# Performance work log

Measured on AMD Instinct MI355X. Metric: run time of the kernel, lower is better.

Reference implementation:

```python
import jax, jax.numpy as jnp
import numpy as np

SIGMA2 = 0.01       # inlier_params[0] -> Scorer_dist sigma2
INLIER_ALPHA = 0.5  # inlier_params[-1]


def setup_inputs() -> dict:
    key = jax.random.key(0)
    k1, k2, k3 = jax.random.split(key, 3)
    B, H, N = 32, 256, 8192
    pts = jax.random.normal(k1, (B, N, 3), dtype=jnp.float32)
    target = jax.random.normal(k2, (B, 3), dtype=jnp.float32)
    sample_idx = jax.random.randint(k3, (B, H, 3), 0, N)
    return {"pts": pts, "target": target, "sample_idx": sample_idx}


def _fit_planes(pts, sample_idx):
    # gather 3 points per hypothesis: pts [B,N,3], sample_idx [B,H,3] -> [B,H,3,3]
    B = pts.shape[0]
    b_idx = jnp.arange(B)[:, None, None]
    tri = pts[b_idx, sample_idx]                     # [B,H,3pts,3coords]
    p0, p1, p2 = tri[:, :, 0], tri[:, :, 1], tri[:, :, 2]
    n = jnp.cross(p1 - p0, p2 - p0)                  # plane normal [B,H,3]
    d = -jnp.sum(n * p0, axis=-1, keepdims=True)     # plane offset [B,H,1]
    planes = jnp.concatenate([n, d], axis=-1)        # [B,H,4]
    # sample_hyp fallback: degenerate (all-zero) planes replaced by ones
    all_zero = jnp.all(planes == 0, axis=-1, keepdims=True)
    planes = jnp.where(all_zero, jnp.ones_like(planes), planes)
    # normalize all 4 components by normal norm
    norm = jnp.sqrt(jnp.sum(planes[..., :3] ** 2, axis=-1, keepdims=True))
    return planes / norm


def reference(pts, target, sample_idx):
    B = pts.shape[0]
    planes = _fit_planes(pts, sample_idx)            # [B,H,4]
    normal = planes[..., :3]
    # Scorer_dist: |n . p + d| over all points, gaussian, sum over points
    dists = jnp.abs(jnp.einsum('bhc,bnc->bhn', normal, pts) + planes[..., 3:4])
    score = jnp.sum(jnp.exp(-(dists ** 2) / (2.0 * SIGMA2)), axis=2)  # [B,H]
    # ms_euclidean loss against target normal (sign-invariant)
    t = target[:, None, :]                           # [B,1,3]
    loss = jnp.minimum(jnp.sum((normal - t) ** 2, axis=2),
                       jnp.sum((normal + t) ** 2, axis=2))            # [B,H]
    maxidx = jnp.argmax(score, axis=1)               # [B]
    top_loss = jnp.take_along_axis(loss, maxidx[:, None], axis=1)[:, 0]
    pred = jnp.take_along_axis(normal, maxidx[:, None, None], axis=1)[:, 0]
    w = jax.nn.softmax(INLIER_ALPHA * score, axis=1)
    exp_loss = jnp.sum(loss * w, axis=1)             # [B]
    return exp_loss, top_loss, pred
```

## Files before the change

### kernel.cpp

```cpp
#include <hip/hip_runtime.h>
#include <math.h>

#define BB 32
#define HH 256
#define NN 8192
#define CC 16
#define CHUNK (NN / CC)
#define P 8
#define SUB (CHUNK / P)

#define WS_LOSS_F ((size_t)BB * HH * 4)
#define WS_PART_F (WS_LOSS_F + (size_t)BB * HH)

__global__ __launch_bounds__(HH) void score_kernel(
    const float* __restrict__ pts, const float* __restrict__ target,
    const int* __restrict__ sidx, float* __restrict__ ws,
    float* __restrict__ partial) {
  const int chunk = blockIdx.x, b = blockIdx.y;
  const int h = threadIdx.x;
  __shared__ float4 smp[CHUNK * 3 / 4];
  __shared__ float4 plane_lds[HH];
  __shared__ float scorepad[HH * 9];

  const float4* src4 =
      (const float4*)(pts + ((long)b * NN + (long)chunk * CHUNK) * 3);
#pragma unroll
  for (int j = h; j < CHUNK * 3 / 4; j += HH) {
    __builtin_amdgcn_global_load_lds(src4 + j, &smp[j], 16, 0, 0);
  }

  long ibase = ((long)b * HH + h) * 3;
  int i0 = sidx[ibase], i1 = sidx[ibase + 1], i2 = sidx[ibase + 2];
  const float* pb = pts + (long)b * NN * 3;
  float p0x = pb[3 * i0], p0y = pb[3 * i0 + 1], p0z = pb[3 * i0 + 2];
  float p1x = pb[3 * i1], p1y = pb[3 * i1 + 1], p1z = pb[3 * i1 + 2];
  float p2x = pb[3 * i2], p2y = pb[3 * i2 + 1], p2z = pb[3 * i2 + 2];
  float v1x = p1x - p0x, v1y = p1y - p0y, v1z = p1z - p0z;
  float v2x = p2x - p0x, v2y = p2y - p0y, v2z = p2z - p0z;
  float nx = __fsub_rn(__fmul_rn(v1y, v2z), __fmul_rn(v1z, v2y));
  float ny = __fsub_rn(__fmul_rn(v1z, v2x), __fmul_rn(v1x, v2z));
  float nz = __fsub_rn(__fmul_rn(v1x, v2y), __fmul_rn(v1y, v2x));
  float d = -(__fmul_rn(nx, p0x) + __fmul_rn(ny, p0y) + __fmul_rn(nz, p0z));
  if (nx == 0.0f && ny == 0.0f && nz == 0.0f && d == 0.0f) {
    nx = 1.0f; ny = 1.0f; nz = 1.0f; d = 1.0f;
  }
  float norm = sqrtf(nx * nx + ny * ny + nz * nz);
  nx /= norm; ny /= norm; nz /= norm; d /= norm;
  plane_lds[h] = make_float4(nx, ny, nz, d);

  if (chunk == 0) {
    ((float4*)ws)[b * HH + h] = make_float4(nx, ny, nz, d);
    float tx = target[b * 3], ty = target[b * 3 + 1], tz = target[b * 3 + 2];
    float lm = (nx - tx) * (nx - tx) + (ny - ty) * (ny - ty) + (nz - tz) * (nz - tz);
    float lp = (nx + tx) * (nx + tx) + (ny + ty) * (ny + ty) + (nz + tz) * (nz + tz);
    ws[WS_LOSS_F + b * HH + h] = fminf(lm, lp);
  }
  __syncthreads();

  const float SC = 8.4932180028801371f;
  const int pid = h & 31;
  const int s = h >> 5;
  float4 pls[P];
#pragma unroll
  for (int k = 0; k < P; ++k) {
    float4 q = plane_lds[pid + (k << 5)];
    pls[k] = make_float4(q.x * SC, q.y * SC, q.z * SC, q.w * SC);
  }

  float acc[P];
#pragma unroll
  for (int k = 0; k < P; ++k) acc[k] = 0.f;
  const int sbase = s * (SUB * 3 / 4);
#pragma unroll 4
  for (int g = 0; g < SUB / 4; ++g) {
    float4 v0 = smp[sbase + 3 * g + 0];
    float4 v1 = smp[sbase + 3 * g + 1];
    float4 v2 = smp[sbase + 3 * g + 2];
#pragma unroll
    for (int k = 0; k < P; ++k) {
      float4 q = pls[k];
      float t0 = fmaf(q.x, v0.x, fmaf(q.y, v0.y, fmaf(q.z, v0.z, q.w)));
      float t1 = fmaf(q.x, v0.w, fmaf(q.y, v1.x, fmaf(q.z, v1.y, q.w)));
      float t2 = fmaf(q.x, v1.z, fmaf(q.y, v1.w, fmaf(q.z, v2.x, q.w)));
      float t3 = fmaf(q.x, v2.y, fmaf(q.y, v2.z, fmaf(q.z, v2.w, q.w)));
      float e0 = __builtin_amdgcn_exp2f(-(t0 * t0));
      float e1 = __builtin_amdgcn_exp2f(-(t1 * t1));
      float e2 = __builtin_amdgcn_exp2f(-(t2 * t2));
      float e3 = __builtin_amdgcn_exp2f(-(t3 * t3));
      acc[k] += (e0 + e1) + (e2 + e3);
    }
  }

#pragma unroll
  for (int k = 0; k < P; ++k) scorepad[(pid + (k << 5)) * 9 + s] = acc[k];
  __syncthreads();
  float rowsum = 0.f;
#pragma unroll
  for (int j = 0; j < P; ++j) rowsum += scorepad[h * 9 + j];
  partial[((long)b * CC + chunk) * HH + h] = rowsum;
}

__global__ __launch_bounds__(HH) void finalize_kernel(
    const float* __restrict__ ws, float* __restrict__ out) {
  int b = blockIdx.x, h = threadIdx.x;
  const float* lossArr = ws + WS_LOSS_F;
  const float* partial = ws + WS_PART_F;
  float s = 0.f;
#pragma unroll
  for (int c = 0; c < CC; ++c) s += partial[((long)b * CC + c) * HH + h];
  float l = lossArr[b * HH + h];

  __shared__ float redv[4];
  __shared__ int redi[4];
  __shared__ float sw[4], swl[4];

  float v = s; int idx = h;
#pragma unroll
  for (int o = 32; o > 0; o >>= 1) {
    float ov = __shfl_xor(v, o);
    int oi = __shfl_xor(idx, o);
    if (ov > v || (ov == v && oi < idx)) { v = ov; idx = oi; }
  }
  const int wid = h >> 6;
  if ((h & 63) == 0) { redv[wid] = v; redi[wid] = idx; }
  __syncthreads();
  float m = redv[0]; int mi = redi[0];
#pragma unroll
  for (int w = 1; w < 4; ++w) {
    float ov = redv[w]; int oi = redi[w];
    if (ov > m || (ov == m && oi < mi)) { m = ov; mi = oi; }
  }

  const float HL = 0.72134752044448170f;
  float wv = __builtin_amdgcn_exp2f(HL * (s - m));
  float wl = wv * l;
#pragma unroll
  for (int o = 32; o > 0; o >>= 1) {
    wv += __shfl_xor(wv, o);
    wl += __shfl_xor(wl, o);
  }
  if ((h & 63) == 0) { sw[wid] = wv; swl[wid] = wl; }
  __syncthreads();
  if (h == 0) {
    float S1 = (sw[0] + sw[1]) + (sw[2] + sw[3]);
    float S2 = (swl[0] + swl[1]) + (swl[2] + swl[3]);
    out[b] = S2 / S1;
    out[BB + b] = lossArr[b * HH + mi];
    float4 p = ((const float4*)ws)[b * HH + mi];
    out[2 * BB + 3 * b + 0] = p.x;
    out[2 * BB + 3 * b + 1] = p.y;
    out[2 * BB + 3 * b + 2] = p.z;
  }
}

extern "C" void kernel_launch(void* const* d_in, const int* in_sizes, int n_in,
                              void* d_out, int out_size, void* d_ws, size_t ws_size,
                              hipStream_t stream) {
  const float* pts = (const float*)d_in[0];
  const float* target = (const float*)d_in[1];
  const int* sidx = (const int*)d_in[2];
  float* out = (float*)d_out;
  float* ws = (float*)d_ws;
  float* partial = ws + WS_PART_F;

  score_kernel<<<dim3(CC, BB), HH, 0, stream>>>(pts, target, sidx, ws, partial);
  finalize_kernel<<<BB, HH, 0, stream>>>(ws, out);
}
```

Baseline: 22.95 us.

## Split hypotheses across blocks and specialize warps for loading vs plane fitting

The grid is repartitioned from 16 point chunks into 8 chunks by 2 hypothesis halves. Each block now scores 128 planes against 1024 points, with P reduced to 4 planes per thread. Within a block, the upper 128 threads issue the async point-to-LDS copies while the lower 128 gather sample points and fit planes, so the two phases overlap. Normalization now uses a reciprocal sqrt instead of sqrt plus divides, which changes rounding slightly. The score accumulation now spans the whole 1024-point chunk per block, which raises the point data loaded per plane and could cost more memory traffic.

```diff
diff --git a/kernel.cpp b/kernel.cpp
--- a/kernel.cpp
+++ b/kernel.cpp
@@ -4,56 +4,67 @@
 #define BB 32
 #define HH 256
 #define NN 8192
-#define CC 16
-#define CHUNK (NN / CC)
-#define P 8
-#define SUB (CHUNK / P)
+#define NC 8
+#define PHALF 2
+#define CHUNK (NN / NC)
+#define PPB (HH / PHALF)
+#define P 4
+#define SUB (CHUNK / 8)
 
 #define WS_LOSS_F ((size_t)BB * HH * 4)
 #define WS_PART_F (WS_LOSS_F + (size_t)BB * HH)
 
-__global__ __launch_bounds__(HH) void score_kernel(
+__global__ __launch_bounds__(256) void score_kernel(
     const float* __restrict__ pts, const float* __restrict__ target,
     const int* __restrict__ sidx, float* __restrict__ ws,
     float* __restrict__ partial) {
-  const int chunk = blockIdx.x, b = blockIdx.y;
+  const int bx = blockIdx.x;
+  const int ph = bx >> 3, chunk = bx & 7;
+  const int b = blockIdx.y;
   const int h = threadIdx.x;
+
   __shared__ float4 smp[CHUNK * 3 / 4];
-  __shared__ float4 plane_lds[HH];
-  __shared__ float scorepad[HH * 9];
+  __shared__ float4 plane_lds[PPB];
+  __shared__ float scorepad[PPB * 9];
 
-  const float4* src4 =
-      (const float4*)(pts + ((long)b * NN + (long)chunk * CHUNK) * 3);
+  if (h >= 128) {
+    const float4* src4 =
+        (const float4*)(pts + ((long)b * NN + (long)chunk * CHUNK) * 3);
+    const int l = h - 128;
 #pragma unroll
-  for (int j = h; j < CHUNK * 3 / 4; j += HH) {
-    __builtin_amdgcn_global_load_lds(src4 + j, &smp[j], 16, 0, 0);
-  }
+    for (int i = 0; i < 6; ++i) {
+      __builtin_amdgcn_global_load_lds(src4 + l + 128 * i, &smp[l + 128 * i],
+                                       16, 0, 0);
+    }
+  } else {
+    long ibase = ((long)b * HH + ph * PPB + h) * 3;
+    int i0 = sidx[ibase], i1 = sidx[ibase + 1], i2 = sidx[ibase + 2];
+    const float* pb = pts + (long)b * NN * 3;
+    float p0x = pb[3 * i0], p0y = pb[3 * i0 + 1], p0z = pb[3 * i0 + 2];
+    float p1x = pb[3 * i1], p1y = pb[3 * i1 + 1], p1z = pb[3 * i1 + 2];
+    float p2x = pb[3 * i2], p2y = pb[3 * i2 + 1], p2z = pb[3 * i2 + 2];
+    float v1x = p1x - p0x, v1y = p1y - p0y, v1z = p1z - p0z;
+    float v2x = p2x - p0x, v2y = p2y - p0y, v2z = p2z - p0z;
+    float nx = __fsub_rn(__fmul_rn(v1y, v2z), __fmul_rn(v1z, v2y));
+    float ny = __fsub_rn(__fmul_rn(v1z, v2x), __fmul_rn(v1x, v2z));
+    float nz = __fsub_rn(__fmul_rn(v1x, v2y), __fmul_rn(v1y, v2x));
+    float d = -(__fmul_rn(nx, p0x) + __fmul_rn(ny, p0y) + __fmul_rn(nz, p0z));
+    if (nx == 0.0f && ny == 0.0f && nz == 0.0f && d == 0.0f) {
+      nx = 1.0f; ny = 1.0f; nz = 1.0f; d = 1.0f;
+    }
+    float inv = __builtin_amdgcn_rsqf(nx * nx + ny * ny + nz * nz);
+    nx *= inv; ny *= inv; nz *= inv; d *= inv;
+    plane_lds[h] = make_float4(nx, ny, nz, d);
 
-  long ibase = ((long)b * HH + h) * 3;
-  int i0 = sidx[ibase], i1 = sidx[ibase + 1], i2 = sidx[ibase + 2];
-  const float* pb = pts + (long)b * NN * 3;
-  float p0x = pb[3 * i0], p0y = pb[3 * i0 + 1], p0z = pb[3 * i0 + 2];
-  float p1x = pb[3 * i1], p1y = pb[3 * i1 + 1], p1z = pb[3 * i1 + 2];
-  float p2x = pb[3 * i2], p2y = pb[3 * i2 + 1], p2z = pb[3 * i2 + 2];
-  float v1x = p1x - p0x, v1y = p1y - p0y, v1z = p1z - p0z;
-  float v2x = p2x - p0x, v2y = p2y - p0y, v2z = p2z - p0z;
-  float nx = __fsub_rn(__fmul_rn(v1y, v2z), __fmul_rn(v1z, v2y));
-  float ny = __fsub_rn(__fmul_rn(v1z, v2x), __fmul_rn(v1x, v2z));
-  float nz = __fsub_rn(__fmul_rn(v1x, v2y), __fmul_rn(v1y, v2x));
-  float d = -(__fmul_rn(nx, p0x) + __fmul_rn(ny, p0y) + __fmul_rn(nz, p0z));
-  if (nx == 0.0f && ny == 0.0f && nz == 0.0f && d == 0.0f) {
-    nx = 1.0f; ny = 1.0f; nz = 1.0f; d = 1.0f;
-  }
-  float norm = sqrtf(nx * nx + ny * ny + nz * nz);
-  nx /= norm; ny /= norm; nz /= norm; d /= norm;
-  plane_lds[h] = make_float4(nx, ny, nz, d);
-
-  if (chunk == 0) {
-    ((float4*)ws)[b * HH + h] = make_float4(nx, ny, nz, d);
-    float tx = target[b * 3], ty = target[b * 3 + 1], tz = target[b * 3 + 2];
-    float lm = (nx - tx) * (nx - tx) + (ny - ty) * (ny - ty) + (nz - tz) * (nz - tz);
-    float lp = (nx + tx) * (nx + tx) + (ny + ty) * (ny + ty) + (nz + tz) * (nz + tz);
-    ws[WS_LOSS_F + b * HH + h] = fminf(lm, lp);
+    if (chunk == 0) {
+      ((float4*)ws)[b * HH + ph * PPB + h] = make_float4(nx, ny, nz, d);
+      float tx = target[b * 3], ty = target[b * 3 + 1], tz = target[b * 3 + 2];
+      float lm = (nx - tx) * (nx - tx) + (ny - ty) * (ny - ty) +
+                 (nz - tz) * (nz - tz);
+      float lp = (nx + tx) * (nx + tx) + (ny + ty) * (ny + ty) +
+                 (nz + tz) * (nz + tz);
+      ws[WS_LOSS_F + b * HH + ph * PPB + h] = fminf(lm, lp);
+    }
   }
   __syncthreads();
 
@@ -94,10 +105,12 @@
 #pragma unroll
   for (int k = 0; k < P; ++k) scorepad[(pid + (k << 5)) * 9 + s] = acc[k];
   __syncthreads();
-  float rowsum = 0.f;
+  if (h < PPB) {
+    float rowsum = 0.f;
 #pragma unroll
-  for (int j = 0; j < P; ++j) rowsum += scorepad[h * 9 + j];
-  partial[((long)b * CC + chunk) * HH + h] = rowsum;
+    for (int j = 0; j < 8; ++j) rowsum += scorepad[h * 9 + j];
+    partial[(((long)b * PHALF + ph) * NC + chunk) * PPB + h] = rowsum;
+  }
 }
 
 __global__ __launch_bounds__(HH) void finalize_kernel(
@@ -105,24 +118,26 @@
   int b = blockIdx.x, h = threadIdx.x;
   const float* lossArr = ws + WS_LOSS_F;
   const float* partial = ws + WS_PART_F;
+  const int ph = h >> 7, idx = h & 127;
   float s = 0.f;
 #pragma unroll
-  for (int c = 0; c < CC; ++c) s += partial[((long)b * CC + c) * HH + h];
+  for (int c = 0; c < NC; ++c)
+    s += partial[(((long)b * PHALF + ph) * NC + c) * PPB + idx];
   float l = lossArr[b * HH + h];
 
   __shared__ float redv[4];
   __shared__ int redi[4];
   __shared__ float sw[4], swl[4];
 
-  float v = s; int idx = h;
+  float v = s; int vidx = h;
 #pragma unroll
   for (int o = 32; o > 0; o >>= 1) {
     float ov = __shfl_xor(v, o);
-    int oi = __shfl_xor(idx, o);
-    if (ov > v || (ov == v && oi < idx)) { v = ov; idx = oi; }
+    int oi = __shfl_xor(vidx, o);
+    if (ov > v || (ov == v && oi < vidx)) { v = ov; vidx = oi; }
   }
   const int wid = h >> 6;
-  if ((h & 63) == 0) { redv[wid] = v; redi[wid] = idx; }
+  if ((h & 63) == 0) { redv[wid] = v; redi[wid] = vidx; }
   __syncthreads();
   float m = redv[0]; int mi = redi[0];
 #pragma unroll
@@ -163,6 +178,7 @@
   float* ws = (float*)d_ws;
   float* partial = ws + WS_PART_F;
 
-  score_kernel<<<dim3(CC, BB), HH, 0, stream>>>(pts, target, sidx, ws, partial);
+  score_kernel<<<dim3(PHALF * NC, BB), 256, 0, stream>>>(pts, target, sidx, ws,
+                                                         partial);
   finalize_kernel<<<BB, HH, 0, stream>>>(ws, out);
 }
```

New measurement: 22.51 us. No clear change (-1.9%).
